# Kernel optimization log

Measured on AMD Instinct MI355X. Metric: run time of the kernel, lower is better.

The kernel has to match this reference:

```python
import jax, jax.numpy as jnp
import numpy as np
from jax import lax

# --- COSMO-SAC constants (defaults from the layer) ---
T = 623.15
Q0 = 79.53
R0 = 66.69
C_HB = 85580.0
RGAS = 8.3144598 / 4184.0
SIG_HB = 0.0084
EPS = 3.667
AEFF = 7.5
EO = 0.0002395
ZC = 10.0
X0 = 0.235
X1 = 1.0 - 0.235
N_SIGMA = 51
N_ITERS = 50


def _deltaw():
    s = np.linspace(-0.025, 0.025, N_SIGMA)
    sigma_m = np.tile(s, (N_SIGMA, 1))          # rows of grid values
    sigma_n = sigma_m.T
    sigma_acc = np.tril(sigma_n) + np.triu(sigma_m, 1)
    sigma_don = np.tril(sigma_m) + np.triu(sigma_n, 1)
    fpol = (EPS - 1.0) / (EPS + 0.5)
    alpha = 0.3 * AEFF ** 1.5 / EO
    alpha_prime = fpol * alpha
    dw = (alpha_prime / 2.0 * (sigma_m + sigma_n) ** 2
          + C_HB * np.maximum(0.0, sigma_acc - SIG_HB) * np.minimum(0.0, sigma_don + SIG_HB))
    return jnp.asarray(dw, jnp.float32)

DELTAW = _deltaw()                       # [51,51]
SSS = jnp.exp(-DELTAW / (RGAS * T))      # [51,51]


def get_Gamma(psigma):
    """50-step fixed-point solve. psigma: [B,51] -> Gamma: [B,51]."""
    AA = SSS[None, :, :] * psigma[:, None, :]   # [B,51,51]
    def step(G, _):
        Gnew = 1.0 / jnp.einsum('bmn,bn->bm', AA, G)
        return (Gnew + G) * 0.5, None
    G, _ = lax.scan(step, jnp.ones_like(psigma), None, length=N_ITERS)
    return G


def setup_inputs() -> dict:
    key = jax.random.key(0)
    k1, k2, k3, k4 = jax.random.split(key, 4)
    B = 32768
    return {
        "input_my_sigma": jax.random.uniform(k1, (B, N_SIGMA), dtype=jnp.float32),
        "v_compound": jax.random.uniform(k2, (B,), dtype=jnp.float32),
        "input_vt_sigma": jax.random.uniform(k3, (B, N_SIGMA, 2), dtype=jnp.float32),
        "v_vt": jax.random.uniform(k4, (B,), dtype=jnp.float32),
    }


def reference(input_my_sigma, v_compound, input_vt_sigma, v_vt):
    my = input_my_sigma                 # [B,51]
    vt = input_vt_sigma[:, :, 1]        # [B,51]
    A0 = jnp.sum(my, axis=1)            # [B]
    A1 = jnp.sum(vt, axis=1)            # [B]

    psigma_mix = (X0 * my + X1 * vt) / (X0 * A0[:, None] + X1 * A1[:, None])
    lnGamma_mix = jnp.log(get_Gamma(psigma_mix))       # [B,51]

    # residual part for component i = 0
    psigma = my / A0[:, None]
    lnGammai = jnp.log(get_Gamma(psigma))              # [B,51]
    lng_resid = A0 / AEFF * jnp.sum(psigma * (lnGamma_mix - lnGammai), axis=1)

    # combinatorial part (Staverman-Guggenheim)
    q0 = A0 / Q0
    q1 = A1 / Q0
    r0 = v_compound / R0
    r1 = v_vt / R0
    xq = X0 * q0 + X1 * q1
    xr = X0 * r0 + X1 * r1
    theta = X0 * q0 / xq
    phi = X0 * r0 / xr
    l0 = ZC / 2.0 * (r0 - q0) - (r0 - 1.0)
    l1 = ZC / 2.0 * (r1 - q1) - (r1 - 1.0)
    xl = X0 * l0 + X1 * l1
    lng_comb = (jnp.log(phi / X0) + ZC / 2.0 * q0 * jnp.log(theta / phi)
                + l0 - phi / X0 * xl)

    return (lng_resid + lng_comb)[:, None]             # [B,1]
```

## Files before the change

### kernel.cpp

```cpp
#include <hip/hip_runtime.h>

typedef __bf16 bf16;
typedef __attribute__((ext_vector_type(4))) bf16 bf16x4;
typedef __attribute__((ext_vector_type(8))) bf16 bf16x8;
typedef __attribute__((ext_vector_type(16))) float f32x16;

namespace {

constexpr double csqrt(double x) {
  double s = x > 1 ? x : 1;
  for (int i = 0; i < 60; ++i) s = 0.5 * (s + x / s);
  return s;
}
constexpr double AP_D =
    ((3.667 - 1.0) / (3.667 + 0.5)) * (0.3 * (7.5 * csqrt(7.5)) / 0.0002395);
constexpr double RGAST_D = (8.3144598 / 4184.0) * 623.15;

__device__ __forceinline__ float sss_val(int i, int j) {
  if (i > 50 || j > 50) return 0.0f;
  const float si = -0.025f + 0.001f * (float)i;
  const float sj = -0.025f + 0.001f * (float)j;
  const float smx = fmaxf(si, sj);
  const float smn = fminf(si, sj);
  const float acc = fmaxf(0.0f, smx - 0.0084f);
  const float don = fminf(0.0f, smn + 0.0084f);
  const float dw = (float)(AP_D * 0.5) * (si + sj) * (si + sj) + 85580.0f * acc * don;
  return expf(-dw * (float)(1.0 / RGAST_D));
}

__device__ __forceinline__ float fast_log(float x) {
  return __builtin_amdgcn_logf(x) * 0.69314718056f;
}

__device__ __forceinline__ f32x16 mfma_bf16(bf16x8 a, bf16x8 b, f32x16 c) {
  return __builtin_amdgcn_mfma_f32_32x32x16_bf16(a, b, c, 0, 0, 0);
}

}

__global__ __launch_bounds__(256, 1) void cosmo_mfma(
    const float* __restrict__ my_sigma,
    const float* __restrict__ v_comp,
    const float* __restrict__ vt_sigma,
    const float* __restrict__ v_vt,
    float* __restrict__ out,
    int B)
{
  __shared__ bf16 lds[4][32 * 68];

  const int lane = threadIdx.x & 63;
  const int wv   = threadIdx.x >> 6;
  const int s    = lane & 31;
  const int hf   = lane >> 5;
  const int e    = (blockIdx.x * 4 + wv) * 16 + (s >> 1);
  const int task = s & 1;
  const bool ein = (e < B);
  const int  ec  = ein ? e : 0;

  float myv[2][16], vtv[2][16];
#pragma unroll
  for (int t = 0; t < 2; ++t)
#pragma unroll
    for (int r = 0; r < 16; ++r) {
      const int n  = 32 * t + (r & 3) + 8 * (r >> 2) + 4 * hf;
      const bool nv = (n < 51);
      const int nc = nv ? n : 50;
      const float a = my_sigma[(size_t)ec * 51 + nc];
      const float b = vt_sigma[((size_t)ec * 51 + nc) * 2 + 1];
      myv[t][r] = nv ? a : 0.0f;
      vtv[t][r] = nv ? b : 0.0f;
    }

  float pA0 = 0.f, pA1 = 0.f;
#pragma unroll
  for (int t = 0; t < 2; ++t)
#pragma unroll
    for (int r = 0; r < 16; ++r) { pA0 += myv[t][r]; pA1 += vtv[t][r]; }
  const float A0 = pA0 + __shfl_xor(pA0, 32, 64);
  const float A1 = pA1 + __shfl_xor(pA1, 32, 64);

  const float den  = task ? (0.235f * A0 + 0.765f * A1) : A0;
  const float rden = __builtin_amdgcn_rcpf(den);
  const float rA0  = __builtin_amdgcn_rcpf(A0);

  float wC[2][16], pp[2][16], G[2][16];
#pragma unroll
  for (int t = 0; t < 2; ++t)
#pragma unroll
    for (int r = 0; r < 16; ++r) {
      const float num = task ? (0.235f * myv[t][r] + 0.765f * vtv[t][r]) : myv[t][r];
      wC[t][r] = num * rden;
      pp[t][r] = myv[t][r] * rA0 * 0.69314718f;
      G[t][r]  = 1.0f;
    }

  bf16x8 afr[2][4];
#pragma unroll
  for (int t = 0; t < 2; ++t)
#pragma unroll
    for (int kt = 0; kt < 4; ++kt) {
      bf16x8 v;
#pragma unroll
      for (int i = 0; i < 8; ++i)
        v[i] = (bf16)sss_val(32 * t + s, kt * 16 + 8 * hf + i);
      afr[t][kt] = v;
    }

  bf16* slab = &lds[wv][0];
  const int wbase = s * 68 + 4 * hf;
  const int rbase = s * 68 + 8 * hf;
  const float vInd = hf ? 1.0f : 0.0f;

#pragma unroll 1
  for (int it = 0; it < 50; ++it) {
#pragma unroll
    for (int t = 0; t < 2; ++t)
#pragma unroll
      for (int q = 0; q < 4; ++q) {
        bf16x4 hv;
#pragma unroll
        for (int r = 0; r < 4; ++r)
          hv[r] = (bf16)(wC[t][q * 4 + r] * G[t][q * 4 + r]);
        *(bf16x4*)(slab + wbase + 32 * t + 8 * q) = hv;
      }

    bf16x8 bfr[4];
#pragma unroll
    for (int kt = 0; kt < 4; ++kt) {
      const bf16x4 lo = *(const bf16x4*)(slab + rbase + 16 * kt);
      const bf16x4 hi = *(const bf16x4*)(slab + rbase + 16 * kt + 4);
      bfr[kt] = __builtin_shufflevector(lo, hi, 0, 1, 2, 3, 4, 5, 6, 7);
    }

    const f32x16 z = {};
    f32x16 acc0 = mfma_bf16(afr[0][0], bfr[0], z);
    f32x16 acc1 = mfma_bf16(afr[1][0], bfr[0], z);
#pragma unroll
    for (int kt = 1; kt < 4; ++kt) {
      acc0 = mfma_bf16(afr[0][kt], bfr[kt], acc0);
      acc1 = mfma_bf16(afr[1][kt], bfr[kt], acc1);
    }

#pragma unroll
    for (int r = 0; r < 16; ++r)
      G[0][r] = 0.5f * (G[0][r] + __builtin_amdgcn_rcpf(acc0[r]));
#pragma unroll
    for (int r = 0; r < 16; ++r) {
      float d = acc1[r];
      const int q = r >> 2;
      if (q == 3)      d += 1.0f;
      else if (q == 2) d += ((r & 3) == 3) ? 1.0f : vInd;
      G[1][r] = 0.5f * (G[1][r] + __builtin_amdgcn_rcpf(d));
    }
  }

  float Sp = 0.f;
#pragma unroll
  for (int t = 0; t < 2; ++t)
#pragma unroll
    for (int r = 0; r < 16; ++r)
      Sp += pp[t][r] * __builtin_amdgcn_logf(G[t][r]);

  const float St = Sp + __shfl_xor(Sp, 32, 64);
  const float So = __shfl_xor(St, 1, 64);

  if (task == 0 && hf == 0 && ein) {
    const float lng_resid = A0 * (1.0f / 7.5f) * (So - St);
    const float v0  = v_comp[e];
    const float v1v = v_vt[e];
    const float q0 = A0 * (1.0f / 79.53f), q1 = A1 * (1.0f / 79.53f);
    const float r0 = v0 * (1.0f / 66.69f), r1 = v1v * (1.0f / 66.69f);
    const float xq = 0.235f * q0 + 0.765f * q1;
    const float xr = 0.235f * r0 + 0.765f * r1;
    const float theta = 0.235f * q0 * __builtin_amdgcn_rcpf(xq);
    const float phi   = 0.235f * r0 * __builtin_amdgcn_rcpf(xr);
    const float l0 = 5.0f * (r0 - q0) - (r0 - 1.0f);
    const float l1 = 5.0f * (r1 - q1) - (r1 - 1.0f);
    const float xl = 0.235f * l0 + 0.765f * l1;
    const float lng_comb = fast_log(phi * (1.0f / 0.235f))
                         + 5.0f * q0 * fast_log(theta * __builtin_amdgcn_rcpf(phi))
                         + l0 - (phi * (1.0f / 0.235f)) * xl;
    out[e] = lng_resid + lng_comb;
  }
}

extern "C" void kernel_launch(void* const* d_in, const int* in_sizes, int n_in,
                              void* d_out, int out_size, void* d_ws, size_t ws_size,
                              hipStream_t stream) {
  const float* my  = (const float*)d_in[0];
  const float* vc  = (const float*)d_in[1];
  const float* vts = (const float*)d_in[2];
  const float* vvt = (const float*)d_in[3];
  float* out = (float*)d_out;
  const int B = in_sizes[1];
  const int grid = (B + 63) / 64;
  cosmo_mfma<<<grid, 256, 0, stream>>>(my, vc, vts, vvt, out, B);
}
```

Baseline: 117.9 us.

## Switch fixed-point solve to 16x16x32 MFMA tiles with fewer registers per lane

Measured after the change: 127.5 us. +8.1%, slower.

```diff
diff --git a/kernel.cpp b/kernel.cpp
--- a/kernel.cpp
+++ b/kernel.cpp
@@ -3,7 +3,7 @@
 typedef __bf16 bf16;
 typedef __attribute__((ext_vector_type(4))) bf16 bf16x4;
 typedef __attribute__((ext_vector_type(8))) bf16 bf16x8;
-typedef __attribute__((ext_vector_type(16))) float f32x16;
+typedef __attribute__((ext_vector_type(4))) float f32x4;
 
 namespace {
 
@@ -20,10 +20,8 @@
   if (i > 50 || j > 50) return 0.0f;
   const float si = -0.025f + 0.001f * (float)i;
   const float sj = -0.025f + 0.001f * (float)j;
-  const float smx = fmaxf(si, sj);
-  const float smn = fminf(si, sj);
-  const float acc = fmaxf(0.0f, smx - 0.0084f);
-  const float don = fminf(0.0f, smn + 0.0084f);
+  const float acc = fmaxf(0.0f, fmaxf(si, sj) - 0.0084f);
+  const float don = fminf(0.0f, fminf(si, sj) + 0.0084f);
   const float dw = (float)(AP_D * 0.5) * (si + sj) * (si + sj) + 85580.0f * acc * don;
   return expf(-dw * (float)(1.0 / RGAST_D));
 }
@@ -32,13 +30,13 @@
   return __builtin_amdgcn_logf(x) * 0.69314718056f;
 }
 
-__device__ __forceinline__ f32x16 mfma_bf16(bf16x8 a, bf16x8 b, f32x16 c) {
-  return __builtin_amdgcn_mfma_f32_32x32x16_bf16(a, b, c, 0, 0, 0);
+__device__ __forceinline__ f32x4 mfma16(bf16x8 a, bf16x8 b, f32x4 c) {
+  return __builtin_amdgcn_mfma_f32_16x16x32_bf16(a, b, c, 0, 0, 0);
 }
 
 }
 
-__global__ __launch_bounds__(256, 1) void cosmo_mfma(
+__global__ __launch_bounds__(256, 4) void cosmo_mfma16(
     const float* __restrict__ my_sigma,
     const float* __restrict__ v_comp,
     const float* __restrict__ vt_sigma,
@@ -46,125 +44,114 @@
     float* __restrict__ out,
     int B)
 {
-  __shared__ bf16 lds[4][32 * 68];
+  __shared__ bf16 lds[4][16 * 72];
 
   const int lane = threadIdx.x & 63;
   const int wv   = threadIdx.x >> 6;
-  const int s    = lane & 31;
-  const int hf   = lane >> 5;
-  const int e    = (blockIdx.x * 4 + wv) * 16 + (s >> 1);
+  const int s    = lane & 15;
+  const int g    = lane >> 4;
+  const int e    = blockIdx.x * 32 + wv * 8 + (s >> 1);
   const int task = s & 1;
   const bool ein = (e < B);
   const int  ec  = ein ? e : 0;
 
-  float myv[2][16], vtv[2][16];
+  float myv[16], vtv[16];
 #pragma unroll
-  for (int t = 0; t < 2; ++t)
+  for (int t = 0; t < 4; ++t)
 #pragma unroll
-    for (int r = 0; r < 16; ++r) {
-      const int n  = 32 * t + (r & 3) + 8 * (r >> 2) + 4 * hf;
-      const bool nv = (n < 51);
-      const int nc = nv ? n : 50;
-      const float a = my_sigma[(size_t)ec * 51 + nc];
-      const float b = vt_sigma[((size_t)ec * 51 + nc) * 2 + 1];
-      myv[t][r] = nv ? a : 0.0f;
-      vtv[t][r] = nv ? b : 0.0f;
+    for (int r = 0; r < 4; ++r) {
+      const int n  = 16 * t + 4 * g + r;
+      const bool nv = (n < 51) && ein;
+      const int nc = (n < 51) ? n : 50;
+      myv[4 * t + r] = nv ? my_sigma[(size_t)ec * 51 + nc] : 0.0f;
+      vtv[4 * t + r] = nv ? vt_sigma[((size_t)ec * 51 + nc) * 2 + 1] : 0.0f;
     }
 
   float pA0 = 0.f, pA1 = 0.f;
 #pragma unroll
-  for (int t = 0; t < 2; ++t)
-#pragma unroll
-    for (int r = 0; r < 16; ++r) { pA0 += myv[t][r]; pA1 += vtv[t][r]; }
-  const float A0 = pA0 + __shfl_xor(pA0, 32, 64);
-  const float A1 = pA1 + __shfl_xor(pA1, 32, 64);
+  for (int i = 0; i < 16; ++i) { pA0 += myv[i]; pA1 += vtv[i]; }
+  float A0 = pA0; A0 += __shfl_xor(A0, 16, 64); A0 += __shfl_xor(A0, 32, 64);
+  float A1 = pA1; A1 += __shfl_xor(A1, 16, 64); A1 += __shfl_xor(A1, 32, 64);
 
   const float den  = task ? (0.235f * A0 + 0.765f * A1) : A0;
   const float rden = __builtin_amdgcn_rcpf(den);
   const float rA0  = __builtin_amdgcn_rcpf(A0);
 
-  float wC[2][16], pp[2][16], G[2][16];
+  float wC[16], G[16];
 #pragma unroll
-  for (int t = 0; t < 2; ++t)
+  for (int i = 0; i < 16; ++i) {
+    const float num = task ? (0.235f * myv[i] + 0.765f * vtv[i]) : myv[i];
+    wC[i] = num * rden;
+    G[i]  = 1.0f;
+  }
+
+  bf16x8 afr[4][2];
 #pragma unroll
-    for (int r = 0; r < 16; ++r) {
-      const float num = task ? (0.235f * myv[t][r] + 0.765f * vtv[t][r]) : myv[t][r];
-      wC[t][r] = num * rden;
-      pp[t][r] = myv[t][r] * rA0 * 0.69314718f;
-      G[t][r]  = 1.0f;
-    }
-
-  bf16x8 afr[2][4];
+  for (int t = 0; t < 4; ++t)
 #pragma unroll
-  for (int t = 0; t < 2; ++t)
-#pragma unroll
-    for (int kt = 0; kt < 4; ++kt) {
+    for (int kt = 0; kt < 2; ++kt) {
       bf16x8 v;
 #pragma unroll
       for (int i = 0; i < 8; ++i)
-        v[i] = (bf16)sss_val(32 * t + s, kt * 16 + 8 * hf + i);
+        v[i] = (bf16)sss_val(16 * t + s, 32 * kt + 8 * g + i);
       afr[t][kt] = v;
     }
 
   bf16* slab = &lds[wv][0];
-  const int wbase = s * 68 + 4 * hf;
-  const int rbase = s * 68 + 8 * hf;
-  const float vInd = hf ? 1.0f : 0.0f;
+  const int wb = s * 72 + 4 * g;
+  const int rb = s * 72 + 8 * g;
+  const float gpad = (g == 0) ? 0.0f : 1.0f;
 
 #pragma unroll 1
   for (int it = 0; it < 50; ++it) {
 #pragma unroll
-    for (int t = 0; t < 2; ++t)
+    for (int t = 0; t < 4; ++t) {
+      bf16x4 hv;
 #pragma unroll
-      for (int q = 0; q < 4; ++q) {
-        bf16x4 hv;
-#pragma unroll
-        for (int r = 0; r < 4; ++r)
-          hv[r] = (bf16)(wC[t][q * 4 + r] * G[t][q * 4 + r]);
-        *(bf16x4*)(slab + wbase + 32 * t + 8 * q) = hv;
-      }
-
-    bf16x8 bfr[4];
-#pragma unroll
-    for (int kt = 0; kt < 4; ++kt) {
-      const bf16x4 lo = *(const bf16x4*)(slab + rbase + 16 * kt);
-      const bf16x4 hi = *(const bf16x4*)(slab + rbase + 16 * kt + 4);
-      bfr[kt] = __builtin_shufflevector(lo, hi, 0, 1, 2, 3, 4, 5, 6, 7);
+      for (int r = 0; r < 4; ++r)
+        hv[r] = (bf16)(wC[4 * t + r] * G[4 * t + r]);
+      *(bf16x4*)(slab + wb + 16 * t) = hv;
     }
 
-    const f32x16 z = {};
-    f32x16 acc0 = mfma_bf16(afr[0][0], bfr[0], z);
-    f32x16 acc1 = mfma_bf16(afr[1][0], bfr[0], z);
+    const bf16x8 bfr0 = *(const bf16x8*)(slab + rb);
+    const bf16x8 bfr1 = *(const bf16x8*)(slab + rb + 32);
+
+    const f32x4 z = {};
+    f32x4 acc[4];
 #pragma unroll
-    for (int kt = 1; kt < 4; ++kt) {
-      acc0 = mfma_bf16(afr[0][kt], bfr[kt], acc0);
-      acc1 = mfma_bf16(afr[1][kt], bfr[kt], acc1);
-    }
+    for (int t = 0; t < 4; ++t) acc[t] = mfma16(afr[t][0], bfr0, z);
+#pragma unroll
+    for (int t = 0; t < 4; ++t) acc[t] = mfma16(afr[t][1], bfr1, acc[t]);
 
 #pragma unroll
-    for (int r = 0; r < 16; ++r)
-      G[0][r] = 0.5f * (G[0][r] + __builtin_amdgcn_rcpf(acc0[r]));
+    for (int t = 0; t < 3; ++t)
 #pragma unroll
-    for (int r = 0; r < 16; ++r) {
-      float d = acc1[r];
-      const int q = r >> 2;
-      if (q == 3)      d += 1.0f;
-      else if (q == 2) d += ((r & 3) == 3) ? 1.0f : vInd;
-      G[1][r] = 0.5f * (G[1][r] + __builtin_amdgcn_rcpf(d));
+      for (int r = 0; r < 4; ++r)
+        G[4 * t + r] = 0.5f * (G[4 * t + r] + __builtin_amdgcn_rcpf(acc[t][r]));
+#pragma unroll
+    for (int r = 0; r < 4; ++r) {
+      const float d = acc[3][r] + ((r < 3) ? gpad : 1.0f);
+      G[12 + r] = 0.5f * (G[12 + r] + __builtin_amdgcn_rcpf(d));
     }
   }
 
   float Sp = 0.f;
 #pragma unroll
-  for (int t = 0; t < 2; ++t)
+  for (int t = 0; t < 4; ++t)
 #pragma unroll
-    for (int r = 0; r < 16; ++r)
-      Sp += pp[t][r] * __builtin_amdgcn_logf(G[t][r]);
-
-  const float St = Sp + __shfl_xor(Sp, 32, 64);
+    for (int r = 0; r < 4; ++r) {
+      const int n = 16 * t + 4 * g + r;
+      if (n < 51) {
+        const float p = (ein ? my_sigma[(size_t)ec * 51 + n] : 0.0f) * rA0;
+        Sp += p * __builtin_amdgcn_logf(G[4 * t + r]);
+      }
+    }
+  Sp += __shfl_xor(Sp, 16, 64);
+  Sp += __shfl_xor(Sp, 32, 64);
+  const float St = Sp * 0.69314718056f;
   const float So = __shfl_xor(St, 1, 64);
 
-  if (task == 0 && hf == 0 && ein) {
+  if (task == 0 && g == 0 && ein) {
     const float lng_resid = A0 * (1.0f / 7.5f) * (So - St);
     const float v0  = v_comp[e];
     const float v1v = v_vt[e];
@@ -193,6 +180,6 @@
   const float* vvt = (const float*)d_in[3];
   float* out = (float*)d_out;
   const int B = in_sizes[1];
-  const int grid = (B + 63) / 64;
-  cosmo_mfma<<<grid, 256, 0, stream>>>(my, vc, vts, vvt, out, B);
+  const int grid = (B + 31) / 32;
+  cosmo_mfma16<<<grid, 256, 0, stream>>>(my, vc, vts, vvt, out, B);
 }
```
